# Performance work log

Measured on AMD Instinct MI355X. Metric: run time of the kernel, lower is better.

The kernel has to match this reference:

```python
import jax, jax.numpy as jnp
import numpy as np

H = 8  # nhead
EPS = 1e-5


def _ln(x, g, b):
    mu = x.mean(-1, keepdims=True)
    var = ((x - mu) ** 2).mean(-1, keepdims=True)
    return (x - mu) / jnp.sqrt(var + EPS) * g + b


def _mha(q_in, kv_in, w_qkv, b_qkv, w_o, b_o, mask):
    # PyTorch nn.MultiheadAttention with packed in_proj: rows [Wq; Wk; Wv], y = x @ W.T + b
    d = q_in.shape[-1]
    hd = d // H
    wq, wk, wv = jnp.split(w_qkv, 3, axis=0)
    bq, bk, bv = jnp.split(b_qkv, 3)
    B, Lq = q_in.shape[0], q_in.shape[1]
    Lk = kv_in.shape[1]
    q = (q_in @ wq.T + bq).reshape(B, Lq, H, hd).transpose(0, 2, 1, 3)
    k = (kv_in @ wk.T + bk).reshape(B, Lk, H, hd).transpose(0, 2, 1, 3)
    v = (kv_in @ wv.T + bv).reshape(B, Lk, H, hd).transpose(0, 2, 1, 3)
    s = jnp.einsum('bhqd,bhkd->bhqk', q, k) * np.float32(1.0 / np.sqrt(hd))
    if mask is not None:
        s = s + mask  # additive causal mask, (Lq, Lk) broadcast
    a = jax.nn.softmax(s, axis=-1)
    o = jnp.einsum('bhqk,bhkd->bhqd', a, v).transpose(0, 2, 1, 3).reshape(B, Lq, d)
    return o @ w_o.T + b_o


def _forward(z, target_ids, tok_emb, pos_emb, lp_w, lp_b, lp_ln_g, lp_ln_b,
             sa_qkv_w, sa_qkv_b, sa_out_w, sa_out_b,
             ca_qkv_w, ca_qkv_b, ca_out_w, ca_out_b,
             ln1_g, ln1_b, ln2_g, ln2_b, ln3_g, ln3_b,
             ff1_w, ff1_b, ff2_w, ff2_b, op_w, op_b):
    B, L = target_ids.shape
    # latent_proj: Linear -> GELU (exact) -> LayerNorm; (B, 1, d) memory
    mem = jax.nn.gelu(z @ lp_w.T + lp_b, approximate=False)
    mem = _ln(mem, lp_ln_g, lp_ln_b)[:, None, :]
    # token + positional embedding
    x = tok_emb[target_ids] + pos_emb[jnp.arange(L)][None, :, :]
    # causal additive mask (upper triangle = -inf)
    causal = jnp.where(jnp.tril(jnp.ones((L, L), dtype=bool)), 0.0, -1e9).astype(x.dtype)
    n_layers = sa_qkv_w.shape[0]
    for i in range(n_layers):  # post-norm TransformerDecoderLayer (norm_first=False)
        x = _ln(x + _mha(x, x, sa_qkv_w[i], sa_qkv_b[i], sa_out_w[i], sa_out_b[i], causal), ln1_g[i], ln1_b[i])
        x = _ln(x + _mha(x, mem, ca_qkv_w[i], ca_qkv_b[i], ca_out_w[i], ca_out_b[i], None), ln2_g[i], ln2_b[i])
        ff = jax.nn.relu(x @ ff1_w[i].T + ff1_b[i]) @ ff2_w[i].T + ff2_b[i]
        x = _ln(x + ff, ln3_g[i], ln3_b[i])
    return x @ op_w.T + op_b  # (B, L, vocab)


def setup_inputs() -> dict:
    B, L, D, LAT, V, NL = 32, 128, 512, 256, 50257, 4
    DF = 4 * D
    key = jax.random.key(0)
    ks = jax.random.split(key, 20)
    s = 0.02
    n = lambda k, shp: jax.random.normal(k, shp, dtype=jnp.float32) * s
    return {
        'z': jax.random.normal(ks[0], (B, LAT), dtype=jnp.float32),
        'target_ids': jax.random.randint(ks[1], (B, L), 0, V),
        'tok_emb': n(ks[2], (V, D)),
        'pos_emb': n(ks[3], (L, D)),
        'lp_w': n(ks[4], (D, LAT)), 'lp_b': jnp.zeros((D,)),
        'lp_ln_g': jnp.ones((D,)), 'lp_ln_b': jnp.zeros((D,)),
        'sa_qkv_w': n(ks[5], (NL, 3 * D, D)), 'sa_qkv_b': jnp.zeros((NL, 3 * D)),
        'sa_out_w': n(ks[6], (NL, D, D)), 'sa_out_b': jnp.zeros((NL, D)),
        'ca_qkv_w': n(ks[7], (NL, 3 * D, D)), 'ca_qkv_b': jnp.zeros((NL, 3 * D)),
        'ca_out_w': n(ks[8], (NL, D, D)), 'ca_out_b': jnp.zeros((NL, D)),
        'ln1_g': jnp.ones((NL, D)), 'ln1_b': jnp.zeros((NL, D)),
        'ln2_g': jnp.ones((NL, D)), 'ln2_b': jnp.zeros((NL, D)),
        'ln3_g': jnp.ones((NL, D)), 'ln3_b': jnp.zeros((NL, D)),
        'ff1_w': n(ks[9], (NL, DF, D)), 'ff1_b': jnp.zeros((NL, DF)),
        'ff2_w': n(ks[10], (NL, D, DF)), 'ff2_b': jnp.zeros((NL, D)),
        'op_w': n(ks[11], (V, D)), 'op_b': jnp.zeros((V,)),
    }


def reference(z, target_ids, tok_emb, pos_emb, lp_w, lp_b, lp_ln_g, lp_ln_b,
              sa_qkv_w, sa_qkv_b, sa_out_w, sa_out_b,
              ca_qkv_w, ca_qkv_b, ca_out_w, ca_out_b,
              ln1_g, ln1_b, ln2_g, ln2_b, ln3_g, ln3_b,
              ff1_w, ff1_b, ff2_w, ff2_b, op_w, op_b):
    return _forward(z, target_ids, tok_emb, pos_emb, lp_w, lp_b, lp_ln_g, lp_ln_b,
                    sa_qkv_w, sa_qkv_b, sa_out_w, sa_out_b,
                    ca_qkv_w, ca_qkv_b, ca_out_w, ca_out_b,
                    ln1_g, ln1_b, ln2_g, ln2_b, ln3_g, ln3_b,
                    ff1_w, ff1_b, ff2_w, ff2_b, op_w, op_b)
```

## Files before the change

kernel.cpp:

```cpp
#include <hip/hip_runtime.h>
#include <math.h>

typedef __attribute__((ext_vector_type(8))) short short8;
typedef __attribute__((ext_vector_type(4))) float f32x4;
typedef __attribute__((ext_vector_type(4))) float f4;
typedef __attribute__((ext_vector_type(4))) unsigned short us4;
typedef unsigned short u16;

#define Bn 32
#define Ln 128
#define Dn 512
#define LATn 256
#define Vn 50257
#define VPAD 50304
#define DFn 2048
#define Hn 8
#define HDn 64

#define GLD(src, dst) __builtin_amdgcn_global_load_lds( \
    (const __attribute__((address_space(1))) unsigned int*)(src), \
    (__attribute__((address_space(3))) unsigned int*)(dst), 16, 0, 0)

__device__ __forceinline__ u16 f2bf(float f) {
  union { float f; unsigned u; } v; v.f = f;
  unsigned r = 0x7FFFu + ((v.u >> 16) & 1u);
  return (u16)((v.u + r) >> 16);
}
__device__ __forceinline__ float bf2f(u16 u) {
  union { unsigned u; float f; } v; v.u = ((unsigned)u) << 16;
  return v.f;
}

__global__ __launch_bounds__(256)
void k_cvt_all(const float* __restrict__ s0, const float* __restrict__ s1,
               const float* __restrict__ s2, const float* __restrict__ s3,
               const float* __restrict__ s4, us4* __restrict__ dst) {
  const int C0 = 786432;
  const int C1 = 1048576;
  const int C2 = 2097152;
  const int C3 = 3145728;
  const int C4 = 9584640;
  const int OPN4 = 6432896;
  int i = blockIdx.x * blockDim.x + threadIdx.x;
  int stride = gridDim.x * blockDim.x;
  for (; i < C4; i += stride) {
    const f4* src; int off; bool valid = true;
    if (i < C0)      { src = (const f4*)s0; off = i; }
    else if (i < C1) { src = (const f4*)s1; off = i - C0; }
    else if (i < C2) { src = (const f4*)s2; off = i - C1; }
    else if (i < C3) { src = (const f4*)s3; off = i - C2; }
    else             { src = (const f4*)s4; off = i - C3; valid = off < OPN4; }
    us4 o;
    if (valid) {
      f4 v = src[off];
      o[0] = f2bf(v[0]); o[1] = f2bf(v[1]); o[2] = f2bf(v[2]); o[3] = f2bf(v[3]);
    } else { o[0] = 0; o[1] = 0; o[2] = 0; o[3] = 0; }
    dst[i] = o;
  }
}

__global__ __launch_bounds__(256)
void k_latent_mem(const float* __restrict__ z, const float* __restrict__ lp_w,
                  const float* __restrict__ lp_b, const float* __restrict__ g,
                  const float* __restrict__ be, float* __restrict__ mem) {
  __shared__ float zs[LATn];
  __shared__ float red[16];
  int b = blockIdx.x, t = threadIdx.x;
  zs[t] = z[b * LATn + t];
  __syncthreads();
  float h[2];
  #pragma unroll
  for (int j = 0; j < 2; j++) {
    int oj = t + j * 256;
    const float* w = lp_w + (size_t)oj * LATn;
    float s0 = 0, s1 = 0, s2 = 0, s3 = 0;
    for (int k = 0; k < LATn; k += 4) {
      s0 += zs[k] * w[k]; s1 += zs[k+1] * w[k+1];
      s2 += zs[k+2] * w[k+2]; s3 += zs[k+3] * w[k+3];
    }
    float x = s0 + s1 + s2 + s3 + lp_b[oj];
    h[j] = 0.5f * x * (1.0f + erff(x * 0.70710678118654752f));
  }
  float sum = h[0] + h[1], sq = h[0]*h[0] + h[1]*h[1];
  for (int off = 32; off; off >>= 1) {
    sum += __shfl_down(sum, off, 64);
    sq  += __shfl_down(sq,  off, 64);
  }
  int lane = t & 63, wid = t >> 6;
  if (!lane) { red[wid] = sum; red[8 + wid] = sq; }
  __syncthreads();
  float ts = red[0] + red[1] + red[2] + red[3];
  float tq = red[8] + red[9] + red[10] + red[11];
  float mu = ts * (1.0f / Dn);
  float var = tq * (1.0f / Dn) - mu * mu;
  float rstd = rsqrtf(fmaxf(var, 0.0f) + 1e-5f);
  #pragma unroll
  for (int j = 0; j < 2; j++) {
    int oj = t + j * 256;
    mem[b * Dn + oj] = (h[j] - mu) * rstd * g[oj] + be[oj];
  }
}

__global__ __launch_bounds__(256)
void k_ca(const float* __restrict__ mem, const float* __restrict__ ca_qkv_w,
          const float* __restrict__ ca_qkv_b, const float* __restrict__ ca_out_w,
          const float* __restrict__ ca_out_b, float* __restrict__ ca_add) {
  int blk = blockIdx.x;
  int i = blk >> 5, b = blk & 31, t = threadIdx.x;
  __shared__ float ms[Dn];
  __shared__ float vs[Dn];
  ms[t] = mem[b * Dn + t];
  ms[t + 256] = mem[b * Dn + t + 256];
  __syncthreads();
  const float* wv = ca_qkv_w + ((size_t)i * 1536 + 1024) * Dn;
  const float* bv = ca_qkv_b + i * 1536 + 1024;
  for (int j = t; j < Dn; j += 256) {
    const float* w = wv + (size_t)j * Dn;
    float s0 = 0, s1 = 0, s2 = 0, s3 = 0;
    for (int k = 0; k < Dn; k += 4) {
      s0 += ms[k]*w[k]; s1 += ms[k+1]*w[k+1]; s2 += ms[k+2]*w[k+2]; s3 += ms[k+3]*w[k+3];
    }
    vs[j] = s0 + s1 + s2 + s3 + bv[j];
  }
  __syncthreads();
  const float* wo = ca_out_w + (size_t)i * Dn * Dn;
  const float* bo = ca_out_b + i * Dn;
  for (int j = t; j < Dn; j += 256) {
    const float* w = wo + (size_t)j * Dn;
    float s0 = 0, s1 = 0, s2 = 0, s3 = 0;
    for (int k = 0; k < Dn; k += 4) {
      s0 += vs[k]*w[k]; s1 += vs[k+1]*w[k+1]; s2 += vs[k+2]*w[k+2]; s3 += vs[k+3]*w[k+3];
    }
    ca_add[((size_t)i * Bn + b) * Dn + j] = s0 + s1 + s2 + s3 + bo[j];
  }
}

__global__ __launch_bounds__(128)
void k_embed(const int* __restrict__ ids, const float* __restrict__ tok,
             const float* __restrict__ pos, u16* __restrict__ Xb) {
  int r = blockIdx.x;
  int l = r & (Ln - 1);
  int id = ids[r];
  int c = threadIdx.x * 4;
  f4 te = *(const f4*)&tok[(size_t)id * Dn + c];
  f4 pe = *(const f4*)&pos[(size_t)l * Dn + c];
  f4 v = te + pe;
  us4 o = { f2bf(v[0]), f2bf(v[1]), f2bf(v[2]), f2bf(v[3]) };
  *(us4*)&Xb[(size_t)r * Dn + c] = o;
}

__global__ __launch_bounds__(128)
void k_add_ln(u16* __restrict__ Xb, const u16* __restrict__ Y,
              const float* __restrict__ g, const float* __restrict__ be) {
  int r = blockIdx.x, t = threadIdx.x;
  int c = t * 4;
  us4 xb = *(const us4*)&Xb[(size_t)r * Dn + c];
  us4 yb = *(const us4*)&Y[(size_t)r * Dn + c];
  f4 v;
  v[0] = bf2f(xb[0]) + bf2f(yb[0]); v[1] = bf2f(xb[1]) + bf2f(yb[1]);
  v[2] = bf2f(xb[2]) + bf2f(yb[2]); v[3] = bf2f(xb[3]) + bf2f(yb[3]);
  float sum = v[0] + v[1] + v[2] + v[3];
  float sq = v[0]*v[0] + v[1]*v[1] + v[2]*v[2] + v[3]*v[3];
  for (int off = 32; off; off >>= 1) {
    sum += __shfl_down(sum, off, 64);
    sq  += __shfl_down(sq,  off, 64);
  }
  __shared__ float red[4];
  int lane = t & 63, w = t >> 6;
  if (!lane) { red[w] = sum; red[2 + w] = sq; }
  __syncthreads();
  sum = red[0] + red[1]; sq = red[2] + red[3];
  float mu = sum * (1.0f / Dn);
  float var = sq * (1.0f / Dn) - mu * mu;
  float rstd = rsqrtf(fmaxf(var, 0.0f) + 1e-5f);
  f4 gg = *(const f4*)&g[c];
  f4 bb = *(const f4*)&be[c];
  f4 o = (v - mu) * rstd * gg + bb;
  us4 ob = { f2bf(o[0]), f2bf(o[1]), f2bf(o[2]), f2bf(o[3]) };
  *(us4*)&Xb[(size_t)r * Dn + c] = ob;
}

__global__ __launch_bounds__(128)
void k_add_ln12(u16* __restrict__ Xb, const u16* __restrict__ Y,
                const float* __restrict__ CA,
                const float* __restrict__ g1, const float* __restrict__ b1,
                const float* __restrict__ g2, const float* __restrict__ b2) {
  int r = blockIdx.x, t = threadIdx.x;
  int c = t * 4;
  __shared__ float red[8];
  int lane = t & 63, w = t >> 6;
  us4 xb = *(const us4*)&Xb[(size_t)r * Dn + c];
  us4 yb = *(const us4*)&Y[(size_t)r * Dn + c];
  f4 v;
  v[0] = bf2f(xb[0]) + bf2f(yb[0]); v[1] = bf2f(xb[1]) + bf2f(yb[1]);
  v[2] = bf2f(xb[2]) + bf2f(yb[2]); v[3] = bf2f(xb[3]) + bf2f(yb[3]);
  float sum = v[0] + v[1] + v[2] + v[3];
  float sq = v[0]*v[0] + v[1]*v[1] + v[2]*v[2] + v[3]*v[3];
  for (int off = 32; off; off >>= 1) {
    sum += __shfl_down(sum, off, 64);
    sq  += __shfl_down(sq,  off, 64);
  }
  if (!lane) { red[w] = sum; red[2 + w] = sq; }
  __syncthreads();
  sum = red[0] + red[1]; sq = red[2] + red[3];
  float mu = sum * (1.0f / Dn);
  float var = sq * (1.0f / Dn) - mu * mu;
  float rstd = rsqrtf(fmaxf(var, 0.0f) + 1e-5f);
  f4 g1v = *(const f4*)&g1[c];
  f4 b1v = *(const f4*)&b1[c];
  f4 o1 = (v - mu) * rstd * g1v + b1v;
  f4 ca = *(const f4*)&CA[(size_t)(r >> 7) * Dn + c];
  f4 v2 = o1 + ca;
  float sum2 = v2[0] + v2[1] + v2[2] + v2[3];
  float sq2 = v2[0]*v2[0] + v2[1]*v2[1] + v2[2]*v2[2] + v2[3]*v2[3];
  for (int off = 32; off; off >>= 1) {
    sum2 += __shfl_down(sum2, off, 64);
    sq2  += __shfl_down(sq2,  off, 64);
  }
  if (!lane) { red[4 + w] = sum2; red[6 + w] = sq2; }
  __syncthreads();
  sum2 = red[4] + red[5]; sq2 = red[6] + red[7];
  float mu2 = sum2 * (1.0f / Dn);
  float var2 = sq2 * (1.0f / Dn) - mu2 * mu2;
  float rstd2 = rsqrtf(fmaxf(var2, 0.0f) + 1e-5f);
  f4 g2v = *(const f4*)&g2[c];
  f4 b2v = *(const f4*)&b2[c];
  f4 o2 = (v2 - mu2) * rstd2 * g2v + b2v;
  us4 ob = { f2bf(o2[0]), f2bf(o2[1]), f2bf(o2[2]), f2bf(o2[3]) };
  *(us4*)&Xb[(size_t)r * Dn + c] = ob;
}

__global__ __launch_bounds__(256, 1)
void k_attn_m(const u16* __restrict__ QKV, u16* __restrict__ Ob) {
  constexpr int QS = 0;
  constexpr int KS = 9216;
  constexpr int SFB = 36864;
  constexpr int VTB = 36864 + 66048;
  constexpr int MXB = VTB + 17408;
  constexpr int LXB = MXB + 1024;
  __shared__ __align__(16) char smem[LXB + 1024];
  u16* U = (u16*)smem;
  float* Sf = (float*)(smem + SFB);
  u16* Vt = (u16*)(smem + VTB);
  float* Mx = (float*)(smem + MXB);
  float* Lx = (float*)(smem + LXB);

  int bh = blockIdx.x, b = bh >> 3, h = bh & 7;
  int tid = threadIdx.x, lane = tid & 63, wid = tid >> 6;
  int r = tid & 127, half = tid >> 7;

  {
    const u16* qk = QKV + (size_t)(b * 128 + r) * 1536 + (half ? 512 : 0) + h * 64;
    u16* dst = U + (half ? KS : QS) + r * 72;
    #pragma unroll
    for (int i = 0; i < 64; i += 8)
      *(short8*)(dst + i) = *(const short8*)(qk + i);
    const u16* vsrc = QKV + (size_t)(b * 128 + r) * 1536 + 1024 + h * 64 + half * 32;
    #pragma unroll
    for (int i = 0; i < 32; i += 8) {
      short8 v = *(const short8*)(vsrc + i);
      #pragma unroll
      for (int j = 0; j < 8; j++)
        Vt[(half * 32 + i + j) * 136 + r] = (u16)v[j];
    }
  }
  __syncthreads();

  int qb = wid * 32;
  int fr = lane & 15, qk8 = (lane >> 4) * 8, qrl = (lane >> 4) * 4;
  f32x4 sacc[2][8] = {};
  #pragma unroll
  for (int s = 0; s < 2; s++) {
    short8 av[2], bv[8];
    #pragma unroll
    for (int mi = 0; mi < 2; mi++)
      av[mi] = *(const short8*)(U + QS + (qb + mi * 16 + fr) * 72 + s * 32 + qk8);
    #pragma unroll
    for (int nj = 0; nj < 8; nj++)
      bv[nj] = *(const short8*)(U + KS + (nj * 16 + fr) * 72 + s * 32 + qk8);
    #pragma unroll
    for (int mi = 0; mi < 2; mi++)
      #pragma unroll
      for (int nj = 0; nj < 8; nj++)
        sacc[mi][nj] = __builtin_amdgcn_mfma_f32_16x16x32_bf16(
            av[mi], bv[nj], sacc[mi][nj], 0, 0, 0);
  }
  #pragma unroll
  for (int mi = 0; mi < 2; mi++)
    #pragma unroll
    for (int nj = 0; nj < 8; nj++)
      #pragma unroll
      for (int g = 0; g < 4; g++) {
        int q = qb + mi * 16 + qrl + g;
        int k = nj * 16 + fr;
        Sf[q * 129 + k] = (k <= q) ? sacc[mi][nj][g] * 0.125f : -1e30f;
      }
  __syncthreads();

  int kr = half * 64;
  float m = -1e30f;
  for (int k = 0; k < 64; k++) m = fmaxf(m, Sf[r * 129 + kr + k]);
  Mx[half * 128 + r] = m;
  __syncthreads();
  float mm = fmaxf(Mx[r], Mx[128 + r]);
  float l = 0.0f;
  for (int k = 0; k < 64; k++) {
    float p = __expf(Sf[r * 129 + kr + k] - mm);
    Sf[r * 129 + kr + k] = p;
    l += p;
  }
  Lx[half * 128 + r] = l;
  __syncthreads();
  float linv = 1.0f / (Lx[r] + Lx[128 + r]);
  #pragma unroll
  for (int kc = 0; kc < 8; kc++) {
    short8 pv;
    #pragma unroll
    for (int j = 0; j < 8; j++)
      pv[j] = (short)f2bf(Sf[r * 129 + kr + kc * 8 + j] * linv);
    *(short8*)(U + r * 136 + kr + kc * 8) = pv;
  }
  __syncthreads();

  f32x4 oacc[2][4] = {};
  #pragma unroll
  for (int ks = 0; ks < 4; ks++) {
    short8 av[2], bv[4];
    #pragma unroll
    for (int mi = 0; mi < 2; mi++)
      av[mi] = *(const short8*)(U + (qb + mi * 16 + fr) * 136 + ks * 32 + qk8);
    #pragma unroll
    for (int nj = 0; nj < 4; nj++)
      bv[nj] = *(const short8*)(Vt + (nj * 16 + fr) * 136 + ks * 32 + qk8);
    #pragma unroll
    for (int mi = 0; mi < 2; mi++)
      #pragma unroll
      for (int nj = 0; nj < 4; nj++)
        oacc[mi][nj] = __builtin_amdgcn_mfma_f32_16x16x32_bf16(
            av[mi], bv[nj], oacc[mi][nj], 0, 0, 0);
  }
  #pragma unroll
  for (int mi = 0; mi < 2; mi++)
    #pragma unroll
    for (int nj = 0; nj < 4; nj++)
      #pragma unroll
      for (int g = 0; g < 4; g++) {
        int q = qb + mi * 16 + qrl + g;
        int d = nj * 16 + fr;
        Ob[(size_t)(b * 128 + q) * 512 + h * 64 + d] = f2bf(oacc[mi][nj][g]);
      }
}

template <int EPI, int BNT>
__global__ __launch_bounds__(256, (BNT == 128 ? 2 : 3))
void k_gemm_bt(const u16* __restrict__ A, const u16* __restrict__ Bw,
               const float* __restrict__ bias, void* __restrict__ Cout,
               int gm, int N, int K, int ldc) {
  constexpr int NREP = BNT / 32;
  constexpr int ASTRIDE = 128 * 64;
  constexpr int BSTRIDE = BNT * 64;
  constexpr int TSTRIDE = BNT + 4;
  constexpr int NLA = 4;
  constexpr int NLB = BNT / 32;
  __shared__ __align__(16) char smem[(ASTRIDE + BSTRIDE) * 4];
  u16* As = (u16*)smem;
  u16* Bs = (u16*)(smem + ASTRIDE * 4);
  float* Ts = (float*)smem;

  int lin = blockIdx.x;
  int bm = lin % gm, bn = lin / gm;
  int tid = threadIdx.x, lane = tid & 63, wid = tid >> 6;
  int wr = wid >> 1, wc = wid & 1;
  int fr = lane & 15, q = lane >> 4;
  f32x4 acc[4][NREP] = {};

  auto stage = [&](int it) {
    int buf = it & 1;
    #pragma unroll
    for (int l = 0; l < NLA; l++) {
      int c = tid + l * 256;
      int row = c >> 3;
      int kcg = (c & 7) ^ (row & 7);
      GLD(A + (size_t)(bm * 128 + row) * K + it * 64 + kcg * 8,
          (char*)(As + buf * ASTRIDE) + c * 16);
    }
    #pragma unroll
    for (int l = 0; l < NLB; l++) {
      int c = tid + l * 256;
      int row = c >> 3;
      int kcg = (c & 7) ^ (row & 7);
      GLD(Bw + (size_t)(bn * BNT + row) * K + it * 64 + kcg * 8,
          (char*)(Bs + buf * BSTRIDE) + c * 16);
    }
  };

  int nt = K >> 6;
  stage(0);
  for (int it = 0; it < nt; ++it) {
    int cur = it & 1;
    if (it + 1 < nt) {
      stage(it + 1);
      if constexpr (BNT == 128) asm volatile("s_waitcnt vmcnt(8)" ::: "memory");
      else                      asm volatile("s_waitcnt vmcnt(6)" ::: "memory");
    } else {
      asm volatile("s_waitcnt vmcnt(0)" ::: "memory");
    }
    __builtin_amdgcn_sched_barrier(0);
    __builtin_amdgcn_s_barrier();
    __builtin_amdgcn_sched_barrier(0);
    short8 av[2][4], bv[2][NREP];
    #pragma unroll
    for (int s = 0; s < 2; s++) {
      #pragma unroll
      for (int mi = 0; mi < 4; mi++) {
        int row = wr * 64 + mi * 16 + fr;
        int phys = (s * 4 + q) ^ (row & 7);
        av[s][mi] = *(const short8*)&As[cur * ASTRIDE + row * 64 + phys * 8];
      }
      #pragma unroll
      for (int nj = 0; nj < NREP; nj++) {
        int row = wc * (BNT / 2) + nj * 16 + fr;
        int phys = (s * 4 + q) ^ (row & 7);
        bv[s][nj] = *(const short8*)&Bs[cur * BSTRIDE + row * 64 + phys * 8];
      }
    }
    #pragma unroll
    for (int s = 0; s < 2; s++)
      #pragma unroll
      for (int mi = 0; mi < 4; mi++)
        #pragma unroll
        for (int nj = 0; nj < NREP; nj++)
          acc[mi][nj] = __builtin_amdgcn_mfma_f32_16x16x32_bf16(
              av[s][mi], bv[s][nj], acc[mi][nj], 0, 0, 0);
    asm volatile("s_waitcnt lgkmcnt(0)" ::: "memory");
    __builtin_amdgcn_sched_barrier(0);
    __builtin_amdgcn_s_barrier();
    __builtin_amdgcn_sched_barrier(0);
  }

  float bb[NREP];
  #pragma unroll
  for (int nj = 0; nj < NREP; nj++) {
    int cg = bn * BNT + wc * (BNT / 2) + nj * 16 + fr;
    bb[nj] = (cg < N) ? bias[cg] : 0.0f;
  }
  int rl0 = (lane >> 4) * 4;
  #pragma unroll
  for (int mi = 0; mi < 4; mi++) {
    #pragma unroll
    for (int nj = 0; nj < NREP; nj++) {
      int colL = wc * (BNT / 2) + nj * 16 + fr;
      #pragma unroll
      for (int r = 0; r < 4; r++)
        Ts[(wr * 16 + rl0 + r) * TSTRIDE + colL] = acc[mi][nj][r] + bb[nj];
    }
    __syncthreads();
    constexpr int ITERS = (32 * BNT) / 256;
    #pragma unroll
    for (int i = 0; i < ITERS; i++) {
      int flat = i * 256 + tid;
      int rowf = flat / BNT, col = flat % BNT;
      float v = Ts[rowf * TSTRIDE + col];
      int row_g = bm * 128 + (rowf >> 4) * 64 + mi * 16 + (rowf & 15);
      int col_g = bn * BNT + col;
      size_t off = (size_t)row_g * ldc + col_g;
      if (EPI == 0) {
        if (col_g < N) ((float*)Cout)[off] = v;
      } else if (EPI == 1) {
        ((u16*)Cout)[off] = f2bf(fmaxf(v, 0.0f));
      } else {
        ((u16*)Cout)[off] = f2bf(v);
      }
    }
    if (mi < 3) __syncthreads();
  }
}

__global__ __launch_bounds__(512, 2)
void k_gemm_v256(const u16* __restrict__ A, const u16* __restrict__ Bw,
                 const float* __restrict__ bias, float* __restrict__ Cout,
                 int gm, int N, int K, int ldc) {
  constexpr int ASTRIDE = 256 * 64;
  constexpr int BSTRIDE = 256 * 64;
  constexpr int TSTRIDE = 256 + 4;
  __shared__ __align__(16) char smem[(ASTRIDE + BSTRIDE) * 4];
  u16* As = (u16*)smem;
  u16* Bs = (u16*)(smem + ASTRIDE * 4);
  float* Ts = (float*)smem;

  int lin = blockIdx.x;
  int bm = lin % gm, bn = lin / gm;
  int tid = threadIdx.x, lane = tid & 63, wid = tid >> 6;
  int wr = wid >> 2, wc = wid & 3;
  int fr = lane & 15, q = lane >> 4;
  f32x4 acc[8][4] = {};

  auto stage = [&](int it) {
    int buf = it & 1;
    #pragma unroll
    for (int l = 0; l < 4; l++) {
      int c = tid + l * 512;
      int row = c >> 3;
      int kcg = (c & 7) ^ (row & 7);
      GLD(A + (size_t)(bm * 256 + row) * K + it * 64 + kcg * 8,
          (char*)(As + buf * ASTRIDE) + c * 16);
    }
    #pragma unroll
    for (int l = 0; l < 4; l++) {
      int c = tid + l * 512;
      int row = c >> 3;
      int rowg = bn * 256 + row;
      if (rowg > VPAD - 1) rowg = VPAD - 1;
      int kcg = (c & 7) ^ (row & 7);
      GLD(Bw + (size_t)rowg * K + it * 64 + kcg * 8,
          (char*)(Bs + buf * BSTRIDE) + c * 16);
    }
  };

  int nt = K >> 6;
  stage(0);
  for (int it = 0; it < nt; ++it) {
    int cur = it & 1;
    if (it + 1 < nt) {
      stage(it + 1);
      asm volatile("s_waitcnt vmcnt(8)" ::: "memory");
    } else {
      asm volatile("s_waitcnt vmcnt(0)" ::: "memory");
    }
    __builtin_amdgcn_sched_barrier(0);
    __builtin_amdgcn_s_barrier();
    __builtin_amdgcn_sched_barrier(0);
    #pragma unroll
    for (int s = 0; s < 2; s++) {
      short8 av[8], bv[4];
      #pragma unroll
      for (int mi = 0; mi < 8; mi++) {
        int row = wr * 128 + mi * 16 + fr;
        int phys = (s * 4 + q) ^ (row & 7);
        av[mi] = *(const short8*)&As[cur * ASTRIDE + row * 64 + phys * 8];
      }
      #pragma unroll
      for (int nj = 0; nj < 4; nj++) {
        int row = wc * 64 + nj * 16 + fr;
        int phys = (s * 4 + q) ^ (row & 7);
        bv[nj] = *(const short8*)&Bs[cur * BSTRIDE + row * 64 + phys * 8];
      }
      #pragma unroll
      for (int mi = 0; mi < 8; mi++)
        #pragma unroll
        for (int nj = 0; nj < 4; nj++)
          acc[mi][nj] = __builtin_amdgcn_mfma_f32_16x16x32_bf16(
              av[mi], bv[nj], acc[mi][nj], 0, 0, 0);
    }
    asm volatile("s_waitcnt lgkmcnt(0)" ::: "memory");
    __builtin_amdgcn_sched_barrier(0);
    __builtin_amdgcn_s_barrier();
    __builtin_amdgcn_sched_barrier(0);
  }

  float bb[4];
  #pragma unroll
  for (int nj = 0; nj < 4; nj++) {
    int cg = bn * 256 + wc * 64 + nj * 16 + fr;
    bb[nj] = (cg < N) ? bias[cg] : 0.0f;
  }
  int rl0 = (lane >> 4) * 4;
  #pragma unroll
  for (int mi = 0; mi < 8; mi++) {
    #pragma unroll
    for (int nj = 0; nj < 4; nj++) {
      int colL = wc * 64 + nj * 16 + fr;
      #pragma unroll
      for (int r = 0; r < 4; r++)
        Ts[(wr * 16 + rl0 + r) * TSTRIDE + colL] = acc[mi][nj][r] + bb[nj];
    }
    __syncthreads();
    #pragma unroll
    for (int i = 0; i < 16; i++) {
      int flat = i * 512 + tid;
      int rowf = flat >> 8, col = flat & 255;
      float v = Ts[rowf * TSTRIDE + col];
      int row_g = bm * 256 + (rowf >> 4) * 128 + mi * 16 + (rowf & 15);
      int col_g = bn * 256 + col;
      if (col_g < N)
        Cout[(size_t)row_g * ldc + col_g] = v;
    }
    if (mi < 7) __syncthreads();
  }
}

extern "C" void kernel_launch(void* const* d_in, const int* in_sizes, int n_in,
                              void* d_out, int out_size, void* d_ws, size_t ws_size,
                              hipStream_t stream) {
  const float* z        = (const float*)d_in[0];
  const int*   ids      = (const int*)d_in[1];
  const float* tok      = (const float*)d_in[2];
  const float* pos      = (const float*)d_in[3];
  const float* lp_w     = (const float*)d_in[4];
  const float* lp_b     = (const float*)d_in[5];
  const float* lp_g     = (const float*)d_in[6];
  const float* lp_be    = (const float*)d_in[7];
  const float* sa_qkv_w = (const float*)d_in[8];
  const float* sa_qkv_b = (const float*)d_in[9];
  const float* sa_out_w = (const float*)d_in[10];
  const float* sa_out_b = (const float*)d_in[11];
  const float* ca_qkv_w = (const float*)d_in[12];
  const float* ca_qkv_b = (const float*)d_in[13];
  const float* ca_out_w = (const float*)d_in[14];
  const float* ca_out_b = (const float*)d_in[15];
  const float* ln1_g    = (const float*)d_in[16];
  const float* ln1_b    = (const float*)d_in[17];
  const float* ln2_g    = (const float*)d_in[18];
  const float* ln2_b    = (const float*)d_in[19];
  const float* ln3_g    = (const float*)d_in[20];
  const float* ln3_b    = (const float*)d_in[21];
  const float* ff1_w    = (const float*)d_in[22];
  const float* ff1_b    = (const float*)d_in[23];
  const float* ff2_w    = (const float*)d_in[24];
  const float* ff2_b    = (const float*)d_in[25];
  const float* op_w     = (const float*)d_in[26];
  const float* op_b     = (const float*)d_in[27];

  char* ws = (char*)d_ws;
  u16*   Yb     = (u16*)(ws + 8388608);
  u16*   QKVb   = (u16*)(ws + 16777216);
  u16*   Xb     = (u16*)(ws + 29360128);
  u16*   Ob     = (u16*)(ws + 33554432);
  u16*   H1b    = (u16*)(ws + 37748736);
  float* mem    = (float*)(ws + 54525952);
  float* ca_add = (float*)(ws + 54657024);
  u16*   Wa     = (u16*)(ws + 55050240);

  u16* Wqkv = Wa;
  u16* Wout = Wa + 3145728;
  u16* Wff1 = Wa + 4194304;
  u16* Wff2 = Wa + 8388608;
  u16* Wop  = Wa + 12582912;

  k_latent_mem<<<Bn, 256, 0, stream>>>(z, lp_w, lp_b, lp_g, lp_be, mem);
  k_ca<<<4 * Bn, 256, 0, stream>>>(mem, ca_qkv_w, ca_qkv_b, ca_out_w, ca_out_b, ca_add);
  k_embed<<<Bn * Ln, 128, 0, stream>>>(ids, tok, pos, Xb);
  k_cvt_all<<<2048, 256, 0, stream>>>(sa_qkv_w, sa_out_w, ff1_w, ff2_w, op_w,
                                      (us4*)Wa);

  const int M = Bn * Ln;
  for (int i = 0; i < 4; i++) {
    k_gemm_bt<2, 128><<<32 * 12, 256, 0, stream>>>(
        Xb, Wqkv + (size_t)i * 1536 * Dn, sa_qkv_b + i * 1536, QKVb, 32, 1536, Dn, 1536);
    k_attn_m<<<Bn * Hn, 256, 0, stream>>>(QKVb, Ob);
    k_gemm_bt<2, 64><<<32 * 8, 256, 0, stream>>>(
        Ob, Wout + (size_t)i * Dn * Dn, sa_out_b + i * Dn, Yb, 32, Dn, Dn, Dn);
    k_add_ln12<<<M, 128, 0, stream>>>(Xb, Yb, ca_add + (size_t)i * Bn * Dn,
                                      ln1_g + i * Dn, ln1_b + i * Dn,
                                      ln2_g + i * Dn, ln2_b + i * Dn);
    k_gemm_bt<1, 128><<<32 * 16, 256, 0, stream>>>(
        Xb, Wff1 + (size_t)i * DFn * Dn, ff1_b + i * DFn, H1b, 32, DFn, Dn, DFn);
    k_gemm_bt<2, 64><<<32 * 8, 256, 0, stream>>>(
        H1b, Wff2 + (size_t)i * Dn * DFn, ff2_b + i * Dn, Yb, 32, Dn, DFn, Dn);
    k_add_ln<<<M, 128, 0, stream>>>(Xb, Yb, ln3_g + i * Dn, ln3_b + i * Dn);
  }

  k_gemm_v256<<<16 * 197, 512, 0, stream>>>(
      Xb, Wop, op_b, (float*)d_out, 16, Vn, Dn, Vn);
}
```

Measured before the change: 795.6 us.

## Halve vocab GEMM K-tile, raise occupancy hint, fuse latent projection into cross-attn

The vocab projection GEMM now stages 32-wide K slices instead of 64, halving its LDS footprint, with matching swizzle and waitcnt adjustments. Its launch bound asks for 4 blocks per CU instead of 2, aiming to improve latency hiding. Separately, the latent-memory MLP+LayerNorm kernel is merged into the cross-attention constant kernel, removing a launch and a global round-trip but recomputing the latent projection once per layer. The higher occupancy target may force heavy register spilling with 128 accumulator floats per thread, and halving the K tile doubles the barriers per unit of work.

```diff
diff --git a/kernel.cpp b/kernel.cpp
--- a/kernel.cpp
+++ b/kernel.cpp
@@ -60,12 +60,18 @@
 }
 
 __global__ __launch_bounds__(256)
-void k_latent_mem(const float* __restrict__ z, const float* __restrict__ lp_w,
-                  const float* __restrict__ lp_b, const float* __restrict__ g,
-                  const float* __restrict__ be, float* __restrict__ mem) {
+void k_ca(const float* __restrict__ z, const float* __restrict__ lp_w,
+          const float* __restrict__ lp_b, const float* __restrict__ lp_g,
+          const float* __restrict__ lp_be,
+          const float* __restrict__ ca_qkv_w, const float* __restrict__ ca_qkv_b,
+          const float* __restrict__ ca_out_w, const float* __restrict__ ca_out_b,
+          float* __restrict__ ca_add) {
+  int blk = blockIdx.x;
+  int i = blk >> 5, b = blk & 31, t = threadIdx.x;
   __shared__ float zs[LATn];
   __shared__ float red[16];
-  int b = blockIdx.x, t = threadIdx.x;
+  __shared__ float ms[Dn];
+  __shared__ float vs[Dn];
   zs[t] = z[b * LATn + t];
   __syncthreads();
   float h[2];
@@ -97,20 +103,8 @@
   #pragma unroll
   for (int j = 0; j < 2; j++) {
     int oj = t + j * 256;
-    mem[b * Dn + oj] = (h[j] - mu) * rstd * g[oj] + be[oj];
-  }
-}
-
-__global__ __launch_bounds__(256)
-void k_ca(const float* __restrict__ mem, const float* __restrict__ ca_qkv_w,
-          const float* __restrict__ ca_qkv_b, const float* __restrict__ ca_out_w,
-          const float* __restrict__ ca_out_b, float* __restrict__ ca_add) {
-  int blk = blockIdx.x;
-  int i = blk >> 5, b = blk & 31, t = threadIdx.x;
-  __shared__ float ms[Dn];
-  __shared__ float vs[Dn];
-  ms[t] = mem[b * Dn + t];
-  ms[t + 256] = mem[b * Dn + t + 256];
+    ms[oj] = (h[j] - mu) * rstd * lp_g[oj] + lp_be[oj];
+  }
   __syncthreads();
   const float* wv = ca_qkv_w + ((size_t)i * 1536 + 1024) * Dn;
   const float* bv = ca_qkv_b + i * 1536 + 1024;
@@ -476,12 +470,12 @@
   }
 }
 
-__global__ __launch_bounds__(512, 2)
+__global__ __launch_bounds__(512, 4)
 void k_gemm_v256(const u16* __restrict__ A, const u16* __restrict__ Bw,
                  const float* __restrict__ bias, float* __restrict__ Cout,
                  int gm, int N, int K, int ldc) {
-  constexpr int ASTRIDE = 256 * 64;
-  constexpr int BSTRIDE = 256 * 64;
+  constexpr int ASTRIDE = 256 * 32;
+  constexpr int BSTRIDE = 256 * 32;
   constexpr int TSTRIDE = 256 + 4;
   __shared__ __align__(16) char smem[(ASTRIDE + BSTRIDE) * 4];
   u16* As = (u16*)smem;
@@ -498,60 +492,57 @@
   auto stage = [&](int it) {
     int buf = it & 1;
     #pragma unroll
-    for (int l = 0; l < 4; l++) {
+    for (int l = 0; l < 2; l++) {
       int c = tid + l * 512;
-      int row = c >> 3;
-      int kcg = (c & 7) ^ (row & 7);
-      GLD(A + (size_t)(bm * 256 + row) * K + it * 64 + kcg * 8,
+      int row = c >> 2;
+      int kcg = (c & 3) ^ (row & 3);
+      GLD(A + (size_t)(bm * 256 + row) * K + it * 32 + kcg * 8,
           (char*)(As + buf * ASTRIDE) + c * 16);
     }
     #pragma unroll
-    for (int l = 0; l < 4; l++) {
+    for (int l = 0; l < 2; l++) {
       int c = tid + l * 512;
-      int row = c >> 3;
+      int row = c >> 2;
       int rowg = bn * 256 + row;
       if (rowg > VPAD - 1) rowg = VPAD - 1;
-      int kcg = (c & 7) ^ (row & 7);
-      GLD(Bw + (size_t)rowg * K + it * 64 + kcg * 8,
+      int kcg = (c & 3) ^ (row & 3);
+      GLD(Bw + (size_t)rowg * K + it * 32 + kcg * 8,
           (char*)(Bs + buf * BSTRIDE) + c * 16);
     }
   };
 
-  int nt = K >> 6;
+  int nt = K >> 5;
   stage(0);
   for (int it = 0; it < nt; ++it) {
     int cur = it & 1;
     if (it + 1 < nt) {
       stage(it + 1);
-      asm volatile("s_waitcnt vmcnt(8)" ::: "memory");
+      asm volatile("s_waitcnt vmcnt(4)" ::: "memory");
     } else {
       asm volatile("s_waitcnt vmcnt(0)" ::: "memory");
     }
     __builtin_amdgcn_sched_barrier(0);
     __builtin_amdgcn_s_barrier();
     __builtin_amdgcn_sched_barrier(0);
-    #pragma unroll
-    for (int s = 0; s < 2; s++) {
-      short8 av[8], bv[4];
-      #pragma unroll
-      for (int mi = 0; mi < 8; mi++) {
-        int row = wr * 128 + mi * 16 + fr;
-        int phys = (s * 4 + q) ^ (row & 7);
-        av[mi] = *(const short8*)&As[cur * ASTRIDE + row * 64 + phys * 8];
-      }
-      #pragma unroll
-      for (int nj = 0; nj < 4; nj++) {
-        int row = wc * 64 + nj * 16 + fr;
-        int phys = (s * 4 + q) ^ (row & 7);
-        bv[nj] = *(const short8*)&Bs[cur * BSTRIDE + row * 64 + phys * 8];
-      }
-      #pragma unroll
-      for (int mi = 0; mi < 8; mi++)
-        #pragma unroll
-        for (int nj = 0; nj < 4; nj++)
-          acc[mi][nj] = __builtin_amdgcn_mfma_f32_16x16x32_bf16(
-              av[mi], bv[nj], acc[mi][nj], 0, 0, 0);
-    }
+    short8 av[8], bv[4];
+    #pragma unroll
+    for (int mi = 0; mi < 8; mi++) {
+      int row = wr * 128 + mi * 16 + fr;
+      int phys = q ^ (row & 3);
+      av[mi] = *(const short8*)&As[cur * ASTRIDE + row * 32 + phys * 8];
+    }
+    #pragma unroll
+    for (int nj = 0; nj < 4; nj++) {
+      int row = wc * 64 + nj * 16 + fr;
+      int phys = q ^ (row & 3);
+      bv[nj] = *(const short8*)&Bs[cur * BSTRIDE + row * 32 + phys * 8];
+    }
+    #pragma unroll
+    for (int mi = 0; mi < 8; mi++)
+      #pragma unroll
+      for (int nj = 0; nj < 4; nj++)
+        acc[mi][nj] = __builtin_amdgcn_mfma_f32_16x16x32_bf16(
+            av[mi], bv[nj], acc[mi][nj], 0, 0, 0);
     asm volatile("s_waitcnt lgkmcnt(0)" ::: "memory");
     __builtin_amdgcn_sched_barrier(0);
     __builtin_amdgcn_s_barrier();
@@ -627,7 +618,6 @@
   u16*   Xb     = (u16*)(ws + 29360128);
   u16*   Ob     = (u16*)(ws + 33554432);
   u16*   H1b    = (u16*)(ws + 37748736);
-  float* mem    = (float*)(ws + 54525952);
   float* ca_add = (float*)(ws + 54657024);
   u16*   Wa     = (u16*)(ws + 55050240);
 
@@ -637,8 +627,8 @@
   u16* Wff2 = Wa + 8388608;
   u16* Wop  = Wa + 12582912;
 
-  k_latent_mem<<<Bn, 256, 0, stream>>>(z, lp_w, lp_b, lp_g, lp_be, mem);
-  k_ca<<<4 * Bn, 256, 0, stream>>>(mem, ca_qkv_w, ca_qkv_b, ca_out_w, ca_out_b, ca_add);
+  k_ca<<<4 * Bn, 256, 0, stream>>>(z, lp_w, lp_b, lp_g, lp_be,
+                                   ca_qkv_w, ca_qkv_b, ca_out_w, ca_out_b, ca_add);
   k_embed<<<Bn * Ln, 128, 0, stream>>>(ids, tok, pos, Xb);
   k_cvt_all<<<2048, 256, 0, stream>>>(sa_qkv_w, sa_out_w, ff1_w, ff2_w, op_w,
                                       (us4*)Wa);
```

Result: slower. 1.830 ms (+130.1%).
